# Optimization experiments

Measured on AMD Instinct MI355X. Metric: run time of the kernel, lower is better.

## Reference

```python
import jax, jax.numpy as jnp
import numpy as np

DIM = 768
HEADS = 12
HEAD_DIM = DIM // HEADS
HIDDEN = int(DIM * 4.0)
EPS = 1e-5


def _layernorm(x, g, b):
    mu = jnp.mean(x, axis=-1, keepdims=True)
    var = jnp.mean(jnp.square(x - mu), axis=-1, keepdims=True)
    return (x - mu) * jax.lax.rsqrt(var + EPS) * g + b


def setup_inputs() -> dict:
    key = jax.random.key(0)
    ks = jax.random.split(key, 8)
    s_in = 1.0 / np.sqrt(DIM)
    s_hid = 1.0 / np.sqrt(HIDDEN)
    return {
        "x": jax.random.normal(ks[0], (2, 2048, DIM), dtype=jnp.float32),
        "ln1_g": jnp.ones((DIM,), jnp.float32),
        "ln1_b": jnp.zeros((DIM,), jnp.float32),
        "w_qkv": jax.random.normal(ks[1], (DIM, 3 * DIM), jnp.float32) * s_in,
        "w_proj": jax.random.normal(ks[2], (DIM, DIM), jnp.float32) * s_in,
        "b_proj": jnp.zeros((DIM,), jnp.float32),
        "ln2_g": jnp.ones((DIM,), jnp.float32),
        "ln2_b": jnp.zeros((DIM,), jnp.float32),
        "w_fc1": jax.random.normal(ks[3], (DIM, HIDDEN), jnp.float32) * s_in,
        "b_fc1": jnp.zeros((HIDDEN,), jnp.float32),
        "w_fc2": jax.random.normal(ks[4], (HIDDEN, DIM), jnp.float32) * s_hid,
        "b_fc2": jnp.zeros((DIM,), jnp.float32),
    }


def reference(x, ln1_g, ln1_b, w_qkv, w_proj, b_proj, ln2_g, ln2_b, w_fc1, b_fc1, w_fc2, b_fc2):
    b, n, c = x.shape
    scale = HEAD_DIM ** -0.5

    # --- attention branch ---
    h = _layernorm(x, ln1_g, ln1_b)
    qkv = (h @ w_qkv).reshape(b, n, 3, HEADS, HEAD_DIM)
    q, k, v = jnp.moveaxis(qkv, 2, 0)          # each [b, n, H, hd]
    attn = jnp.einsum("bqhd,bkhd->bhqk", q, k) * scale
    attn = jax.nn.softmax(attn, axis=-1)       # [b, H, n, n] (naive, materialized)
    o = jnp.einsum("bhqk,bkhd->bqhd", attn, v).reshape(b, n, c)
    x = x + o @ w_proj + b_proj

    # --- MLP branch ---
    h2 = _layernorm(x, ln2_g, ln2_b)
    m = jax.nn.gelu(h2 @ w_fc1 + b_fc1, approximate=False)
    x = x + m @ w_fc2 + b_fc2
    return x
```

## Files before the change

kernel.cpp:

```cpp
#include <hip/hip_runtime.h>
#include <math.h>


typedef unsigned short u16;
typedef __attribute__((ext_vector_type(8))) short short8;
typedef __attribute__((ext_vector_type(4))) float f32x4;

#define TOKENS 4096
#define DIM    768
#define QKV_N  2304
#define HID    3072
#define NSEQ   2048
#define NHEAD  12
#define HDIM   64

__device__ __forceinline__ float bf2f(u16 u) {
  union { unsigned i; float f; } v; v.i = ((unsigned)u) << 16; return v.f;
}
__device__ __forceinline__ u16 f2bf(float f) {
  union { float f; unsigned i; } v; v.f = f;
  unsigned r = v.i + 0x7fffu + ((v.i >> 16) & 1u);
  return (u16)(r >> 16);
}
__device__ __forceinline__ u16 f2bf_trunc(float f) {
  union { float f; unsigned i; } v; v.f = f;
  return (u16)(v.i >> 16);
}

__device__ __forceinline__ void async_copy16(const u16* g, u16* l) {
  __builtin_amdgcn_global_load_lds(
      (const __attribute__((address_space(1))) unsigned int*)(unsigned long long)g,
      (__attribute__((address_space(3))) unsigned int*)(unsigned int)(unsigned long long)l,
      16, 0, 0);
}

__global__ __launch_bounds__(256) void prep_kernel(
    const float* __restrict__ x, const float* __restrict__ g,
    const float* __restrict__ b, u16* __restrict__ h,
    const float* __restrict__ in0, u16* __restrict__ out0,
    const float* __restrict__ in1, u16* __restrict__ out1,
    const float* __restrict__ in2, u16* __restrict__ out2,
    const float* __restrict__ in3, u16* __restrict__ out3) {
  const int tid = threadIdx.x;
  if (blockIdx.x < 1024) {
    int wave = tid >> 6, lane = tid & 63;
    int token = blockIdx.x * 4 + wave;
    float v[12];
    const float4* xr = (const float4*)(x + (size_t)token * DIM);
#pragma unroll
    for (int w = 0; w < 3; w++) {
      float4 q = xr[lane + w * 64];
      v[w * 4 + 0] = q.x; v[w * 4 + 1] = q.y; v[w * 4 + 2] = q.z; v[w * 4 + 3] = q.w;
    }
    float s = 0.f;
#pragma unroll
    for (int i = 0; i < 12; i++) s += v[i];
#pragma unroll
    for (int off = 32; off > 0; off >>= 1) s += __shfl_xor(s, off);
    float mu = s * (1.0f / DIM);
    float ss = 0.f;
#pragma unroll
    for (int i = 0; i < 12; i++) { float d = v[i] - mu; ss += d * d; }
#pragma unroll
    for (int off = 32; off > 0; off >>= 1) ss += __shfl_xor(ss, off);
    float rs = rsqrtf(ss * (1.0f / DIM) + 1e-5f);
    ushort4* orow = (ushort4*)(h + (size_t)token * DIM);
    const float4* g4 = (const float4*)g;
    const float4* b4 = (const float4*)b;
#pragma unroll
    for (int w = 0; w < 3; w++) {
      float4 gq = g4[lane + w * 64], bq = b4[lane + w * 64];
      ushort4 o;
      o.x = f2bf((v[w * 4 + 0] - mu) * rs * gq.x + bq.x);
      o.y = f2bf((v[w * 4 + 1] - mu) * rs * gq.y + bq.y);
      o.z = f2bf((v[w * 4 + 2] - mu) * rs * gq.z + bq.z);
      o.w = f2bf((v[w * 4 + 3] - mu) * rs * gq.w + bq.w);
      orow[lane + w * 64] = o;
    }
    return;
  }
  __shared__ u16 t[32][33];
  int bid = blockIdx.x - 1024, rem;
  const float* in; u16* out; int R, C;
  if (bid < 1728)      { in = in0; out = out0; R = 768;  C = 2304; rem = bid; }
  else if (bid < 2304) { in = in1; out = out1; R = 768;  C = 768;  rem = bid - 1728; }
  else if (bid < 4608) { in = in2; out = out2; R = 768;  C = 3072; rem = bid - 2304; }
  else                 { in = in3; out = out3; R = 3072; C = 768;  rem = bid - 4608; }
  int c0 = (rem % (C / 32)) * 32, r0 = (rem / (C / 32)) * 32;
  int tx = tid & 31, ty = tid >> 5;
#pragma unroll
  for (int i = 0; i < 4; i++)
    t[ty + i * 8][tx] = f2bf(in[(size_t)(r0 + ty + i * 8) * C + c0 + tx]);
  __syncthreads();
#pragma unroll
  for (int i = 0; i < 4; i++)
    out[(size_t)(c0 + ty + i * 8) * R + r0 + tx] = t[tx][ty + i * 8];
}

__global__ __launch_bounds__(256) void ln_kernel(const u16* __restrict__ xin,
                                                 const float* __restrict__ g,
                                                 const float* __restrict__ b,
                                                 u16* __restrict__ out) {
  int wave = threadIdx.x >> 6, lane = threadIdx.x & 63;
  int token = blockIdx.x * 4 + wave;
  float v[12];
  const ushort4* xr = (const ushort4*)(xin + (size_t)token * DIM);
#pragma unroll
  for (int w = 0; w < 3; w++) {
    ushort4 q = xr[lane + w * 64];
    v[w * 4 + 0] = bf2f(q.x); v[w * 4 + 1] = bf2f(q.y);
    v[w * 4 + 2] = bf2f(q.z); v[w * 4 + 3] = bf2f(q.w);
  }
  float s = 0.f;
#pragma unroll
  for (int i = 0; i < 12; i++) s += v[i];
#pragma unroll
  for (int off = 32; off > 0; off >>= 1) s += __shfl_xor(s, off);
  float mu = s * (1.0f / DIM);
  float ss = 0.f;
#pragma unroll
  for (int i = 0; i < 12; i++) { float d = v[i] - mu; ss += d * d; }
#pragma unroll
  for (int off = 32; off > 0; off >>= 1) ss += __shfl_xor(ss, off);
  float rs = rsqrtf(ss * (1.0f / DIM) + 1e-5f);

  ushort4* orow = (ushort4*)(out + (size_t)token * DIM);
  const float4* g4 = (const float4*)g;
  const float4* b4 = (const float4*)b;
#pragma unroll
  for (int w = 0; w < 3; w++) {
    float4 gq = g4[lane + w * 64], bq = b4[lane + w * 64];
    ushort4 o;
    o.x = f2bf((v[w * 4 + 0] - mu) * rs * gq.x + bq.x);
    o.y = f2bf((v[w * 4 + 1] - mu) * rs * gq.y + bq.y);
    o.z = f2bf((v[w * 4 + 2] - mu) * rs * gq.z + bq.z);
    o.w = f2bf((v[w * 4 + 3] - mu) * rs * gq.w + bq.w);
    orow[lane + w * 64] = o;
  }
}

template <int BM, int BN, int EPI>
__global__ __launch_bounds__(256, 3) void gemm_bt(
    const u16* __restrict__ A, const u16* __restrict__ BT,
    void* __restrict__ Cout, const float* __restrict__ bias,
    const void* __restrict__ resid, int M, int N, int K,
    u16* __restrict__ vtb) {
  constexpr int MT = BM / 32, NT = BN / 32;
  constexpr int ACH = BM / 16;
  constexpr int CPW = (BM + BN) / 64;
  __shared__ __align__(16) u16 Alds[2][BM * 32];
  __shared__ __align__(16) u16 Blds[2][BN * 32];
  const int tid = threadIdx.x;
  const int lane = tid & 63, wave = tid >> 6;
  const int wr = wave >> 1, wc = wave & 1;
  const int nby = M / BM;
  const int by = blockIdx.x % nby, bx = blockIdx.x / nby;
  const int bm = by * BM, bn = bx * BN;
  const int c16 = lane & 15, quad = lane >> 4;
  const int l4 = lane >> 2, lc = (lane & 3) * 8;

  f32x4 acc[MT][NT];
#pragma unroll
  for (int i = 0; i < MT; i++)
#pragma unroll
    for (int j = 0; j < NT; j++) acc[i][j] = (f32x4){0.f, 0.f, 0.f, 0.f};

  const u16* gsrc[CPW];
  u16* ldst[CPW];
  int hstep[CPW];
#pragma unroll
  for (int c = 0; c < CPW; c++) {
    int chunk = wave * CPW + c;
    if (chunk < ACH) {
      gsrc[c] = A + (size_t)(bm + chunk * 16 + l4) * K + lc;
      ldst[c] = Alds[0] + chunk * 512;
      hstep[c] = BM * 32;
    } else {
      int bc = chunk - ACH;
      gsrc[c] = BT + (size_t)(bn + bc * 16 + l4) * K + lc;
      ldst[c] = Blds[0] + bc * 512;
      hstep[c] = BN * 32;
    }
  }

  for (int kk = 0; kk < K; kk += 64) {
    __syncthreads();
#pragma unroll
    for (int c = 0; c < CPW; c++) {
      async_copy16(gsrc[c] + kk, ldst[c]);
      async_copy16(gsrc[c] + kk + 32, ldst[c] + hstep[c]);
    }
    __syncthreads();
#pragma unroll
    for (int ks = 0; ks < 2; ks++) {
      short8 af[MT], bfr[NT];
#pragma unroll
      for (int mt = 0; mt < MT; mt++)
        af[mt] = *(const short8*)(Alds[ks] + (wr * (BM / 2) + mt * 16 + c16) * 32 + quad * 8);
#pragma unroll
      for (int nt = 0; nt < NT; nt++)
        bfr[nt] = *(const short8*)(Blds[ks] + (wc * (BN / 2) + nt * 16 + c16) * 32 + quad * 8);
#pragma unroll
      for (int mt = 0; mt < MT; mt++)
#pragma unroll
        for (int nt = 0; nt < NT; nt++)
          acc[mt][nt] = __builtin_amdgcn_mfma_f32_16x16x32_bf16(af[mt], bfr[nt],
                                                                acc[mt][nt], 0, 0, 0);
    }
  }

#pragma unroll
  for (int mt = 0; mt < MT; mt++) {
#pragma unroll
    for (int nt = 0; nt < NT; nt++) {
      int col = bn + wc * (BN / 2) + nt * 16 + c16;
      float bv = (EPI != 0) ? bias[col] : 0.f;
      int row0 = bm + wr * (BM / 2) + mt * 16 + quad * 4;
      if (EPI == 0 && col >= 2 * DIM) {
        int b = row0 >> 11;
        ushort4 pk;
        pk.x = f2bf(acc[mt][nt][0]); pk.y = f2bf(acc[mt][nt][1]);
        pk.z = f2bf(acc[mt][nt][2]); pk.w = f2bf(acc[mt][nt][3]);
        *(ushort4*)(vtb + ((size_t)b * DIM + col - 2 * DIM) * NSEQ + (row0 & 2047)) = pk;
        continue;
      }
#pragma unroll
      for (int r = 0; r < 4; r++) {
        int row = row0 + r;
        float vv = acc[mt][nt][r];
        if (EPI == 1) {
          vv += bv + ((const float*)resid)[(size_t)row * N + col];
          ((u16*)Cout)[(size_t)row * N + col] = f2bf(vv);
        } else if (EPI == 2) {
          vv += bv;
          vv = 0.5f * vv * (1.0f + erff(vv * 0.70710678118654752f));
          ((u16*)Cout)[(size_t)row * N + col] = f2bf(vv);
        } else if (EPI == 3) {
          vv += bv + bf2f(((const u16*)resid)[(size_t)row * N + col]);
          ((float*)Cout)[(size_t)row * N + col] = vv;
        } else {
          ((u16*)Cout)[(size_t)row * N + col] = f2bf(vv);
        }
      }
    }
  }
}

__global__ __launch_bounds__(256) void attn_kernel(const u16* __restrict__ qkv,
                                                   const u16* __restrict__ vt,
                                                   u16* __restrict__ o) {
  const int tid = threadIdx.x;
  const int lane = tid & 63, wave = tid >> 6;
  const int c16 = lane & 15, quad = lane >> 4;
  const int bh = blockIdx.x % (2 * NHEAD);
  const int qt = blockIdx.x / (2 * NHEAD);
  const int bb = bh / NHEAD, h = bh % NHEAD;
  __shared__ __align__(16) u16 Klds[2][64 * 64];
  __shared__ __align__(16) u16 Vtlds[2][64 * 64];
  __shared__ __align__(16) u16 Plds[4][16 * 64];
  const size_t base = (size_t)bb * NSEQ * QKV_N;
  const int q0 = qt * 64 + wave * 16;

  const u16* qp = qkv + base + (size_t)(q0 + c16) * QKV_N + h * HDIM;
  short8 qf0 = *(const short8*)(qp + quad * 8);
  short8 qf1 = *(const short8*)(qp + 32 + quad * 8);

  float Ls[4] = {0.f, 0.f, 0.f, 0.f};
  f32x4 Of[4];
#pragma unroll
  for (int dt = 0; dt < 4; dt++) Of[dt] = (f32x4){0.f, 0.f, 0.f, 0.f};

  const int srow = lane >> 3;
  const int schunk = (lane & 7) ^ srow;
  const int r0 = wave * 16;
  const u16* ksrc = qkv + base + (size_t)(r0 + srow) * QKV_N + DIM + h * HDIM + schunk * 8;
  const u16* vsrc = vt + ((size_t)bh * HDIM + r0 + srow) * NSEQ + schunk * 8;

  const int cswz0 = (quad ^ (c16 & 7)) * 8;
  const int cswz1 = ((quad + 4) ^ (c16 & 7)) * 8;
  const float SC = 0.18033688011112042f;

#pragma unroll
  for (int j = 0; j < 2; j++) {
    async_copy16(ksrc + (size_t)(8 * j) * QKV_N, Klds[0] + r0 * 64 + 8 * j * 64);
    async_copy16(vsrc + (size_t)(8 * j) * NSEQ, Vtlds[0] + r0 * 64 + 8 * j * 64);
  }

  for (int it = 0; it < NSEQ / 64; it++) {
    const int cur = it & 1;
    __syncthreads();
    if (it + 1 < NSEQ / 64) {
      const int kt1 = (it + 1) * 64;
      u16* kd = Klds[cur ^ 1] + r0 * 64;
      u16* vd = Vtlds[cur ^ 1] + r0 * 64;
#pragma unroll
      for (int j = 0; j < 2; j++) {
        async_copy16(ksrc + (size_t)(kt1 + 8 * j) * QKV_N, kd + 8 * j * 64);
        async_copy16(vsrc + (size_t)(8 * j) * NSEQ + kt1, vd + 8 * j * 64);
      }
    }

    f32x4 S[4];
#pragma unroll
    for (int nt = 0; nt < 4; nt++) {
      S[nt] = (f32x4){0.f, 0.f, 0.f, 0.f};
      const u16* krow = Klds[cur] + (nt * 16 + c16) * 64;
      short8 ka = *(const short8*)(krow + cswz0);
      short8 kb = *(const short8*)(krow + cswz1);
      S[nt] = __builtin_amdgcn_mfma_f32_16x16x32_bf16(qf0, ka, S[nt], 0, 0, 0);
      S[nt] = __builtin_amdgcn_mfma_f32_16x16x32_bf16(qf1, kb, S[nt], 0, 0, 0);
    }

    u16* pl = Plds[wave];
    const int el = c16 & 7, ch = c16 >> 3;
#pragma unroll
    for (int r = 0; r < 4; r++) {
      float p0 = __builtin_amdgcn_exp2f(S[0][r] * SC);
      float p1 = __builtin_amdgcn_exp2f(S[1][r] * SC);
      float p2 = __builtin_amdgcn_exp2f(S[2][r] * SC);
      float p3 = __builtin_amdgcn_exp2f(S[3][r] * SC);
      Ls[r] += (p0 + p1) + (p2 + p3);
      u16* pr = pl + (quad * 4 + r) * 64;
      const int r7 = (quad * 4 + r) & 7;
      pr[((0 + ch) ^ r7) * 8 + el] = f2bf_trunc(p0);
      pr[((2 + ch) ^ r7) * 8 + el] = f2bf_trunc(p1);
      pr[((4 + ch) ^ r7) * 8 + el] = f2bf_trunc(p2);
      pr[((6 + ch) ^ r7) * 8 + el] = f2bf_trunc(p3);
    }

    short8 pf0 = *(const short8*)(pl + c16 * 64 + cswz0);
    short8 pf1 = *(const short8*)(pl + c16 * 64 + cswz1);
#pragma unroll
    for (int dt = 0; dt < 4; dt++) {
      const u16* vrow = Vtlds[cur] + (dt * 16 + c16) * 64;
      short8 va = *(const short8*)(vrow + cswz0);
      short8 vb = *(const short8*)(vrow + cswz1);
      Of[dt] = __builtin_amdgcn_mfma_f32_16x16x32_bf16(pf0, va, Of[dt], 0, 0, 0);
      Of[dt] = __builtin_amdgcn_mfma_f32_16x16x32_bf16(pf1, vb, Of[dt], 0, 0, 0);
    }
  }

#pragma unroll
  for (int r = 0; r < 4; r++) {
    float t = Ls[r];
    t += __shfl_xor(t, 1); t += __shfl_xor(t, 2);
    t += __shfl_xor(t, 4); t += __shfl_xor(t, 8);
    Ls[r] = t;
  }

#pragma unroll
  for (int dt = 0; dt < 4; dt++)
#pragma unroll
    for (int r = 0; r < 4; r++) {
      int token = q0 + quad * 4 + r;
      float val = Of[dt][r] / Ls[r];
      o[(size_t)(bb * NSEQ + token) * DIM + h * HDIM + dt * 16 + c16] = f2bf(val);
    }
}

extern "C" void kernel_launch(void* const* d_in, const int* in_sizes, int n_in,
                              void* d_out, int out_size, void* d_ws, size_t ws_size,
                              hipStream_t stream) {
  (void)in_sizes; (void)n_in; (void)out_size; (void)ws_size;
  const float* x      = (const float*)d_in[0];
  const float* ln1_g  = (const float*)d_in[1];
  const float* ln1_b  = (const float*)d_in[2];
  const float* w_qkv  = (const float*)d_in[3];
  const float* w_proj = (const float*)d_in[4];
  const float* b_proj = (const float*)d_in[5];
  const float* ln2_g  = (const float*)d_in[6];
  const float* ln2_b  = (const float*)d_in[7];
  const float* w_fc1  = (const float*)d_in[8];
  const float* b_fc1  = (const float*)d_in[9];
  const float* w_fc2  = (const float*)d_in[10];
  const float* b_fc2  = (const float*)d_in[11];
  float* out = (float*)d_out;

  char* p = (char*)d_ws;
  u16* h_bf   = (u16*)p; p += (size_t)TOKENS * DIM * 2;
  u16* qkv_bf = (u16*)p; p += (size_t)TOKENS * QKV_N * 2;
  u16* o_bf   = (u16*)p; p += (size_t)TOKENS * DIM * 2;
  u16* x1_bf  = (u16*)p; p += (size_t)TOKENS * DIM * 2;
  u16* wprojT = (u16*)p; p += (size_t)DIM * DIM * 2;
  u16* wfc1T  = (u16*)p; p += (size_t)HID * DIM * 2;
  u16* wfc2T  = (u16*)p; p += (size_t)DIM * HID * 2;
  u16* wqkvT  = (u16*)p; p += (size_t)QKV_N * DIM * 2;
  u16* vtb    = (u16*)p; p += (size_t)TOKENS * DIM * 2;
  u16* m_bf   = qkv_bf;

  prep_kernel<<<dim3(1024 + 6912), 256, 0, stream>>>(
      x, ln1_g, ln1_b, h_bf,
      w_qkv, wqkvT, w_proj, wprojT, w_fc1, wfc1T, w_fc2, wfc2T);

  gemm_bt<64, 128, 0><<<dim3((QKV_N / 128) * (TOKENS / 64)), 256, 0, stream>>>(
      h_bf, wqkvT, qkv_bf, nullptr, nullptr, TOKENS, QKV_N, DIM, vtb);
  attn_kernel<<<dim3(2 * NHEAD * (NSEQ / 64)), 256, 0, stream>>>(qkv_bf, vtb, o_bf);
  gemm_bt<64, 128, 1><<<dim3((DIM / 128) * (TOKENS / 64)), 256, 0, stream>>>(
      o_bf, wprojT, x1_bf, b_proj, x, TOKENS, DIM, DIM, nullptr);
  ln_kernel<<<TOKENS / 4, 256, 0, stream>>>(x1_bf, ln2_g, ln2_b, h_bf);
  gemm_bt<128, 128, 2><<<dim3((HID / 128) * (TOKENS / 128)), 256, 0, stream>>>(
      h_bf, wfc1T, m_bf, b_fc1, nullptr, TOKENS, HID, DIM, nullptr);
  gemm_bt<64, 128, 3><<<dim3((DIM / 128) * (TOKENS / 64)), 256, 0, stream>>>(
      m_bf, wfc2T, out, b_fc2, x1_bf, TOKENS, DIM, HID, nullptr);
}
```

Measured before the change: 269.0 us.

## Split attention waves 2x2 over query and key halves with cross-wave reduction

```diff
diff --git a/kernel.cpp b/kernel.cpp
--- a/kernel.cpp
+++ b/kernel.cpp
@@ -5,6 +5,7 @@
 typedef unsigned short u16;
 typedef __attribute__((ext_vector_type(8))) short short8;
 typedef __attribute__((ext_vector_type(4))) float f32x4;
+typedef __attribute__((ext_vector_type(2))) unsigned int uint2v;
 
 #define TOKENS 4096
 #define DIM    768
@@ -25,6 +26,10 @@
 __device__ __forceinline__ u16 f2bf_trunc(float f) {
   union { float f; unsigned i; } v; v.f = f;
   return (u16)(v.i >> 16);
+}
+__device__ __forceinline__ unsigned pack_bf2(float a, float b) {
+  union { float f; unsigned i; } x, y; x.f = a; y.f = b;
+  return (x.i >> 16) | (y.i & 0xffff0000u);
 }
 
 __device__ __forceinline__ void async_copy16(const u16* g, u16* l) {
@@ -246,39 +251,48 @@
   }
 }
 
-__global__ __launch_bounds__(256) void attn_kernel(const u16* __restrict__ qkv,
-                                                   const u16* __restrict__ vt,
-                                                   u16* __restrict__ o) {
+__global__ __launch_bounds__(256, 3) void attn_kernel(const u16* __restrict__ qkv,
+                                                      const u16* __restrict__ vt,
+                                                      u16* __restrict__ o) {
   const int tid = threadIdx.x;
   const int lane = tid & 63, wave = tid >> 6;
   const int c16 = lane & 15, quad = lane >> 4;
+  const int wq = wave >> 1, wk = wave & 1;
   const int bh = blockIdx.x % (2 * NHEAD);
   const int qt = blockIdx.x / (2 * NHEAD);
   const int bb = bh / NHEAD, h = bh % NHEAD;
   __shared__ __align__(16) u16 Klds[2][64 * 64];
   __shared__ __align__(16) u16 Vtlds[2][64 * 64];
-  __shared__ __align__(16) u16 Plds[4][16 * 64];
+  __shared__ __align__(16) u16 Plds[4][32 * 32];
   const size_t base = (size_t)bb * NSEQ * QKV_N;
-  const int q0 = qt * 64 + wave * 16;
-
-  const u16* qp = qkv + base + (size_t)(q0 + c16) * QKV_N + h * HDIM;
-  short8 qf0 = *(const short8*)(qp + quad * 8);
-  short8 qf1 = *(const short8*)(qp + 32 + quad * 8);
-
-  float Ls[4] = {0.f, 0.f, 0.f, 0.f};
-  f32x4 Of[4];
-#pragma unroll
-  for (int dt = 0; dt < 4; dt++) Of[dt] = (f32x4){0.f, 0.f, 0.f, 0.f};
+  const int q0 = qt * 64;
+  const int sw = c16 & 7;
+
+  short8 qf[2][2];
+#pragma unroll
+  for (int qs = 0; qs < 2; qs++) {
+    const u16* qp = qkv + base + (size_t)(q0 + wq * 32 + qs * 16 + c16) * QKV_N + h * HDIM;
+    qf[qs][0] = *(const short8*)(qp + quad * 8);
+    qf[qs][1] = *(const short8*)(qp + 32 + quad * 8);
+  }
+
+  float Ls[2] = {0.f, 0.f};
+  f32x4 Of[2][4];
+#pragma unroll
+  for (int qs = 0; qs < 2; qs++)
+#pragma unroll
+    for (int dt = 0; dt < 4; dt++) Of[qs][dt] = (f32x4){0.f, 0.f, 0.f, 0.f};
 
   const int srow = lane >> 3;
   const int schunk = (lane & 7) ^ srow;
   const int r0 = wave * 16;
   const u16* ksrc = qkv + base + (size_t)(r0 + srow) * QKV_N + DIM + h * HDIM + schunk * 8;
   const u16* vsrc = vt + ((size_t)bh * HDIM + r0 + srow) * NSEQ + schunk * 8;
-
-  const int cswz0 = (quad ^ (c16 & 7)) * 8;
-  const int cswz1 = ((quad + 4) ^ (c16 & 7)) * 8;
   const float SC = 0.18033688011112042f;
+
+  u16* pl = Plds[wave];
+  const int psw = (c16 >> 2) & 3;
+  const int pq = quad >> 1, ph = (quad & 1) * 4;
 
 #pragma unroll
   for (int j = 0; j < 2; j++) {
@@ -300,62 +314,103 @@
       }
     }
 
-    f32x4 S[4];
-#pragma unroll
-    for (int nt = 0; nt < 4; nt++) {
-      S[nt] = (f32x4){0.f, 0.f, 0.f, 0.f};
-      const u16* krow = Klds[cur] + (nt * 16 + c16) * 64;
-      short8 ka = *(const short8*)(krow + cswz0);
-      short8 kb = *(const short8*)(krow + cswz1);
-      S[nt] = __builtin_amdgcn_mfma_f32_16x16x32_bf16(qf0, ka, S[nt], 0, 0, 0);
-      S[nt] = __builtin_amdgcn_mfma_f32_16x16x32_bf16(qf1, kb, S[nt], 0, 0, 0);
-    }
-
-    u16* pl = Plds[wave];
-    const int el = c16 & 7, ch = c16 >> 3;
-#pragma unroll
-    for (int r = 0; r < 4; r++) {
-      float p0 = __builtin_amdgcn_exp2f(S[0][r] * SC);
-      float p1 = __builtin_amdgcn_exp2f(S[1][r] * SC);
-      float p2 = __builtin_amdgcn_exp2f(S[2][r] * SC);
-      float p3 = __builtin_amdgcn_exp2f(S[3][r] * SC);
-      Ls[r] += (p0 + p1) + (p2 + p3);
-      u16* pr = pl + (quad * 4 + r) * 64;
-      const int r7 = (quad * 4 + r) & 7;
-      pr[((0 + ch) ^ r7) * 8 + el] = f2bf_trunc(p0);
-      pr[((2 + ch) ^ r7) * 8 + el] = f2bf_trunc(p1);
-      pr[((4 + ch) ^ r7) * 8 + el] = f2bf_trunc(p2);
-      pr[((6 + ch) ^ r7) * 8 + el] = f2bf_trunc(p3);
-    }
-
-    short8 pf0 = *(const short8*)(pl + c16 * 64 + cswz0);
-    short8 pf1 = *(const short8*)(pl + c16 * 64 + cswz1);
+    short8 kf0[2], kf1[2];
+#pragma unroll
+    for (int kt = 0; kt < 2; kt++) {
+      const u16* krow = Klds[cur] + (wk * 32 + kt * 16 + c16) * 64;
+      kf0[kt] = *(const short8*)(krow + (quad ^ sw) * 8);
+      kf1[kt] = *(const short8*)(krow + ((quad + 4) ^ sw) * 8);
+    }
+
+    f32x4 St[2][2];
+#pragma unroll
+    for (int qs = 0; qs < 2; qs++)
+#pragma unroll
+      for (int kt = 0; kt < 2; kt++) {
+        f32x4 s = (f32x4){0.f, 0.f, 0.f, 0.f};
+        s = __builtin_amdgcn_mfma_f32_16x16x32_bf16(kf0[kt], qf[qs][0], s, 0, 0, 0);
+        s = __builtin_amdgcn_mfma_f32_16x16x32_bf16(kf1[kt], qf[qs][1], s, 0, 0, 0);
+        St[qs][kt] = s;
+      }
+
+    short8 vf[4];
 #pragma unroll
     for (int dt = 0; dt < 4; dt++) {
       const u16* vrow = Vtlds[cur] + (dt * 16 + c16) * 64;
-      short8 va = *(const short8*)(vrow + cswz0);
-      short8 vb = *(const short8*)(vrow + cswz1);
-      Of[dt] = __builtin_amdgcn_mfma_f32_16x16x32_bf16(pf0, va, Of[dt], 0, 0, 0);
-      Of[dt] = __builtin_amdgcn_mfma_f32_16x16x32_bf16(pf1, vb, Of[dt], 0, 0, 0);
-    }
-  }
-
-#pragma unroll
-  for (int r = 0; r < 4; r++) {
-    float t = Ls[r];
-    t += __shfl_xor(t, 1); t += __shfl_xor(t, 2);
-    t += __shfl_xor(t, 4); t += __shfl_xor(t, 8);
-    Ls[r] = t;
-  }
-
-#pragma unroll
-  for (int dt = 0; dt < 4; dt++)
-#pragma unroll
-    for (int r = 0; r < 4; r++) {
-      int token = q0 + quad * 4 + r;
-      float val = Of[dt][r] / Ls[r];
-      o[(size_t)(bb * NSEQ + token) * DIM + h * HDIM + dt * 16 + c16] = f2bf(val);
-    }
+      vf[dt] = *(const short8*)(vrow + ((wk * 4 + quad) ^ sw) * 8);
+    }
+
+#pragma unroll
+    for (int qs = 0; qs < 2; qs++) {
+      const int row = qs * 16 + c16;
+      u16* prow = pl + row * 32 + ph;
+      float a = 0.f;
+#pragma unroll
+      for (int kt = 0; kt < 2; kt++) {
+        float p0 = __builtin_amdgcn_exp2f(St[qs][kt][0] * SC);
+        float p1 = __builtin_amdgcn_exp2f(St[qs][kt][1] * SC);
+        float p2 = __builtin_amdgcn_exp2f(St[qs][kt][2] * SC);
+        float p3 = __builtin_amdgcn_exp2f(St[qs][kt][3] * SC);
+        a += (p0 + p1) + (p2 + p3);
+        uint2v pk;
+        pk.x = pack_bf2(p0, p1);
+        pk.y = pack_bf2(p2, p3);
+        *(uint2v*)(prow + ((kt * 2 + pq) ^ psw) * 8) = pk;
+      }
+      Ls[qs] += a;
+    }
+
+    short8 pf[2];
+#pragma unroll
+    for (int qs = 0; qs < 2; qs++)
+      pf[qs] = *(const short8*)(pl + (qs * 16 + c16) * 32 + (quad ^ psw) * 8);
+#pragma unroll
+    for (int dt = 0; dt < 4; dt++)
+#pragma unroll
+      for (int qs = 0; qs < 2; qs++)
+        Of[qs][dt] = __builtin_amdgcn_mfma_f32_16x16x32_bf16(pf[qs], vf[dt],
+                                                             Of[qs][dt], 0, 0, 0);
+  }
+
+  __syncthreads();
+  float* red = (float*)&Klds[0][0];
+  float* lred = (float*)&Plds[0][0];
+  if (wk == 1) {
+    float* dst = red + wq * 2048;
+#pragma unroll
+    for (int qs = 0; qs < 2; qs++)
+#pragma unroll
+      for (int dt = 0; dt < 4; dt++)
+        *(f32x4*)(dst + (qs * 4 + dt) * 256 + lane * 4) = Of[qs][dt];
+    lred[wq * 128 + lane] = Ls[0];
+    lred[wq * 128 + 64 + lane] = Ls[1];
+  }
+  __syncthreads();
+  if (wk == 0) {
+    const float* src = red + wq * 2048;
+#pragma unroll
+    for (int qs = 0; qs < 2; qs++)
+#pragma unroll
+      for (int dt = 0; dt < 4; dt++)
+        Of[qs][dt] += *(const f32x4*)(src + (qs * 4 + dt) * 256 + lane * 4);
+    float t0 = Ls[0] + lred[wq * 128 + lane];
+    float t1 = Ls[1] + lred[wq * 128 + 64 + lane];
+    t0 += __shfl_xor(t0, 16); t0 += __shfl_xor(t0, 32);
+    t1 += __shfl_xor(t1, 16); t1 += __shfl_xor(t1, 32);
+#pragma unroll
+    for (int qs = 0; qs < 2; qs++) {
+      float tq = qs ? t1 : t0;
+#pragma unroll
+      for (int r = 0; r < 4; r++) {
+        float L = __shfl(tq, quad * 4 + r);
+        int token = q0 + wq * 32 + qs * 16 + quad * 4 + r;
+        u16* orow = o + (size_t)(bb * NSEQ + token) * DIM + h * HDIM;
+#pragma unroll
+        for (int dt = 0; dt < 4; dt++)
+          orow[dt * 16 + c16] = f2bf(Of[qs][dt][r] / L);
+      }
+    }
+  }
 }
 
 extern "C" void kernel_launch(void* const* d_in, const int* in_sizes, int n_in,
```

New measurement: 256.8 us. 4.5% less time.
